# Performance work log

Hardware: AMD Instinct MI355X
Metric: run time of the kernel (lower is better)

Reference implementation:

```python
import jax, jax.numpy as jnp
import numpy as np

B, T, D, H = 512, 512, 128, 128


def setup_inputs() -> dict:
    key = jax.random.key(0)
    k1, k2, k3 = jax.random.split(key, 3)
    bound = 1.0 / np.sqrt(D)  # kaiming_uniform with a=sqrt(5) on [D,H]
    inp = {
        "input": jax.random.normal(k1, (B, T, D), dtype=jnp.float32),
        "mask": jnp.ones((B, T), dtype=jnp.int32),
        "Wt": jax.random.uniform(k2, (D, H), jnp.float32, -bound, bound),
        "Wx": jax.random.uniform(k3, (D, H), jnp.float32, -bound, bound),
        "rate": jnp.zeros((1,), jnp.float32) + 0.8,
    }
    return inp


def reference(input, mask, Wt, Wx, rate):
    b, t, d = input.shape
    # time decays: [t-1, t-2, ..., 0] + 1  -> shape [t]
    b_time_decays = jnp.arange(t - 1, -1, -1, dtype=input.dtype) + 1.0  # [T]

    # get_last_visit: pick features at last valid (mask==1) timestep per batch
    last_idx = jnp.sum(mask, axis=1).astype(jnp.int32) - 1            # [B]
    last_visit = jnp.take_along_axis(input, last_idx[:, None, None], axis=1)[:, 0]  # [B,D]

    q = last_visit @ Wt                                   # [B,H]
    k = jnp.einsum('btd,dh->bth', input, Wx)              # [B,T,H]
    dot_product = jnp.einsum('bh,bth->bt', q, k)          # [B,T]

    sig = jax.nn.sigmoid(dot_product)
    denominator = jax.nn.sigmoid(rate) * (
        jnp.log(2.72 + (1.0 - sig)) * b_time_decays[None, :]
    )
    e = jax.nn.relu(sig / denominator)

    e = jnp.where(mask == 0, -1e9, e)
    a = jax.nn.softmax(e, axis=1)                         # [B,T]
    v = jnp.einsum('bt,btd->bd', a, input)                # [B,D]
    return v, a
```

## Files before the change

kernel.cpp:

```cpp
#include <hip/hip_runtime.h>
#include <math.h>

constexpr int Bn = 512;
constexpr int Tn = 512;
constexpr int Dn = 128;
constexpr int Hn = 128;

__device__ __forceinline__ float rowsum16(float x) {
    int v;
    v = __float_as_int(x);
    x += __int_as_float(__builtin_amdgcn_update_dpp(0, v, 0x121, 0xF, 0xF, true));
    v = __float_as_int(x);
    x += __int_as_float(__builtin_amdgcn_update_dpp(0, v, 0x122, 0xF, 0xF, true));
    v = __float_as_int(x);
    x += __int_as_float(__builtin_amdgcn_update_dpp(0, v, 0x124, 0xF, 0xF, true));
    v = __float_as_int(x);
    x += __int_as_float(__builtin_amdgcn_update_dpp(0, v, 0x128, 0xF, 0xF, true));
    return x;
}

__global__ __launch_bounds__(128)
void compute_u_kernel(const float* __restrict__ input,
                      const int*   __restrict__ mask,
                      const float* __restrict__ Wt,
                      const float* __restrict__ Wx,
                      float* __restrict__ ws_u)
{
    const int b   = blockIdx.x;
    const int tid = threadIdx.x;
    const float* __restrict__ inb = input + (size_t)b * Tn * Dn;

    __shared__ float lvs[Dn];
    __shared__ float qs[Hn];
    __shared__ int   ired[2];

    const int4 m4 = ((const int4*)(mask + (size_t)b * Tn))[tid];
    int ms = m4.x + m4.y + m4.z + m4.w;
    #pragma unroll
    for (int off = 32; off > 0; off >>= 1) ms += __shfl_down(ms, off, 64);
    if ((tid & 63) == 0) ired[tid >> 6] = ms;
    __syncthreads();
    const int last_idx = ired[0] + ired[1] - 1;

    lvs[tid] = inb[(size_t)last_idx * Dn + tid];
    __syncthreads();

    float q = 0.f;
    #pragma unroll 16
    for (int d = 0; d < Dn; ++d) q = fmaf(lvs[d], Wt[d * Hn + tid], q);
    qs[tid] = q;
    __syncthreads();

    float u = 0.f;
    const float* wxr = Wx + tid * Hn;
    #pragma unroll 16
    for (int h = 0; h < Hn; ++h) u = fmaf(wxr[h], qs[h], u);
    ws_u[b * Dn + tid] = u;
}

constexpr int NT2 = 512;
constexpr int NW2 = NT2 / 64;
constexpr int HR  = Tn / 2;
constexpr int SW  = HR / 32;

__global__ __launch_bounds__(NT2, 4)
void attn_stream2(const float* __restrict__ input,
                  const int*   __restrict__ mask,
                  const float* __restrict__ ws_u,
                  const float* __restrict__ rate,
                  float* __restrict__ vpart,
                  float* __restrict__ lpart,
                  float* __restrict__ out_a)
{
    const int j    = blockIdx.x;
    const int b    = j >> 1;
    const int half = j & 1;
    const int tid  = threadIdx.x;
    const int lane = tid & 63;
    const int wid  = tid >> 6;
    const int seg  = tid & 15;
    const int rg   = tid >> 4;
    const int rbase = half * HR;
    const float4* __restrict__ in4 = (const float4*)(input + (size_t)b * Tn * Dn);

    __shared__ int   msk[HR];
    __shared__ float redl[NW2];
    __shared__ float vp[32 * 132];

    if (tid < HR) msk[tid] = mask[(size_t)b * Tn + rbase + tid];
    const float4 u4a = ((const float4*)(ws_u + b * Dn))[seg * 2];
    const float4 u4b = ((const float4*)(ws_u + b * Dn))[seg * 2 + 1];
    const float srate = 1.f / (1.f + __expf(-rate[0]));
    __syncthreads();

    float4 v0 = make_float4(0.f, 0.f, 0.f, 0.f);
    float4 v1 = make_float4(0.f, 0.f, 0.f, 0.f);
    float  lsum = 0.f;

    #pragma unroll
    for (int s = 0; s < SW; ++s) {
        const int rl  = s * 32 + rg;
        const int row = rbase + rl;
        const float4 x0 = in4[row * 32 + seg * 2];
        const float4 x1 = in4[row * 32 + seg * 2 + 1];
        float dot = x0.x * u4a.x + x0.y * u4a.y + x0.z * u4a.z + x0.w * u4a.w;
        dot = fmaf(x1.x, u4b.x, dot);
        dot = fmaf(x1.y, u4b.y, dot);
        dot = fmaf(x1.z, u4b.z, dot);
        dot = fmaf(x1.w, u4b.w, dot);
        dot = rowsum16(dot);
        const float sig = 1.f / (1.f + __expf(-dot));
        const float den = srate * (__logf(2.72f + (1.f - sig)) * (float)(Tn - row));
        const float e   = fmaxf(sig / den, 0.f);
        const float p   = msk[rl] ? __expf(e) : 0.f;
        v0.x = fmaf(p, x0.x, v0.x);
        v0.y = fmaf(p, x0.y, v0.y);
        v0.z = fmaf(p, x0.z, v0.z);
        v0.w = fmaf(p, x0.w, v0.w);
        v1.x = fmaf(p, x1.x, v1.x);
        v1.y = fmaf(p, x1.y, v1.y);
        v1.z = fmaf(p, x1.z, v1.z);
        v1.w = fmaf(p, x1.w, v1.w);
        if (seg == 0) { out_a[(size_t)b * Tn + row] = p; lsum += p; }
    }

    {
        float* vr = vp + rg * 132 + seg * 8;
        ((float4*)vr)[0] = v0;
        ((float4*)vr)[1] = v1;
    }
    float ls = lsum;
    #pragma unroll
    for (int off = 32; off > 0; off >>= 1) ls += __shfl_down(ls, off, 64);
    if (lane == 0) redl[wid] = ls;
    __syncthreads();

    if (tid < Dn) {
        float s = 0.f;
        #pragma unroll
        for (int r = 0; r < 32; ++r) s += vp[r * 132 + tid];
        vpart[(size_t)j * Dn + tid] = s;
    }
    if (tid == 0) {
        float l = 0.f;
        #pragma unroll
        for (int w = 0; w < NW2; ++w) l += redl[w];
        lpart[j] = l;
    }
}

__global__ __launch_bounds__(512)
void attn_finish(const float* __restrict__ vpart,
                 const float* __restrict__ lpart,
                 float* __restrict__ out_v,
                 float* __restrict__ out_a)
{
    const int b   = blockIdx.x;
    const int tid = threadIdx.x;
    const float invl = 1.f / (lpart[2 * b] + lpart[2 * b + 1]);
    out_a[(size_t)b * Tn + tid] *= invl;
    if (tid < Dn)
        out_v[(size_t)b * Dn + tid] =
            (vpart[(size_t)(2 * b) * Dn + tid] + vpart[(size_t)(2 * b + 1) * Dn + tid]) * invl;
}

extern "C" void kernel_launch(void* const* d_in, const int* in_sizes, int n_in,
                              void* d_out, int out_size, void* d_ws, size_t ws_size,
                              hipStream_t stream) {
    const float* input = (const float*)d_in[0];
    const int*   mask  = (const int*)d_in[1];
    const float* Wt    = (const float*)d_in[2];
    const float* Wx    = (const float*)d_in[3];
    const float* rate  = (const float*)d_in[4];

    float* out   = (float*)d_out;
    float* out_v = out;
    float* out_a = out + Bn * Dn;

    float* ws_u  = (float*)d_ws;
    float* vpart = ws_u + (size_t)Bn * Dn;
    float* lpart = vpart + (size_t)2 * Bn * Dn;

    compute_u_kernel<<<Bn, 128, 0, stream>>>(input, mask, Wt, Wx, ws_u);
    attn_stream2<<<2 * Bn, NT2, 0, stream>>>(input, mask, ws_u, rate, vpart, lpart, out_a);
    attn_finish<<<Bn, 512, 0, stream>>>(vpart, lpart, out_v, out_a);
}
```

Before: 37.60 us.

## Stream input rows into LDS via async global_load_lds with triple buffering

Replaces direct per-thread global float4 loads in the attention streaming kernel with asynchronous global-to-LDS loads. Each wave gets its own triple-buffered ring of 4-row chunks, managed with explicit vmcnt waits, so memory traffic overlaps with compute. Attention probabilities are staged in LDS and written to global in one coalesced pass at the end. The LDS footprint grows (about 48KB of staging per block), which may reduce occupancy at 4 blocks per CU, and the hand-written waitcnt sequencing is fragile.

```diff
diff --git a/kernel.cpp b/kernel.cpp
--- a/kernel.cpp
+++ b/kernel.cpp
@@ -58,34 +58,40 @@
     ws_u[b * Dn + tid] = u;
 }
 
-constexpr int NT2 = 512;
-constexpr int NW2 = NT2 / 64;
-constexpr int HR  = Tn / 2;
-constexpr int SW  = HR / 32;
+constexpr int NT2    = 512;
+constexpr int NW2    = NT2 / 64;
+constexpr int HR     = Tn / 2;
+constexpr int RPW    = HR / NW2;
+constexpr int CHROWS = 4;
+constexpr int NCH    = RPW / CHROWS;
+constexpr int CB     = 3;
+constexpr int CHB    = CHROWS * Dn * 4;
 
 __global__ __launch_bounds__(NT2, 4)
-void attn_stream2(const float* __restrict__ input,
-                  const int*   __restrict__ mask,
-                  const float* __restrict__ ws_u,
-                  const float* __restrict__ rate,
-                  float* __restrict__ vpart,
-                  float* __restrict__ lpart,
-                  float* __restrict__ out_a)
+void attn_stream_dma(const float* __restrict__ input,
+                     const int*   __restrict__ mask,
+                     const float* __restrict__ ws_u,
+                     const float* __restrict__ rate,
+                     float* __restrict__ vpart,
+                     float* __restrict__ lpart,
+                     float* __restrict__ out_a)
 {
-    const int j    = blockIdx.x;
-    const int b    = j >> 1;
-    const int half = j & 1;
-    const int tid  = threadIdx.x;
-    const int lane = tid & 63;
-    const int wid  = tid >> 6;
-    const int seg  = tid & 15;
-    const int rg   = tid >> 4;
+    const int j     = blockIdx.x;
+    const int b     = j >> 1;
+    const int half  = j & 1;
+    const int tid   = threadIdx.x;
+    const int lane  = tid & 63;
+    const int w     = tid >> 6;
+    const int seg   = lane & 15;
+    const int rslot = lane >> 4;
     const int rbase = half * HR;
-    const float4* __restrict__ in4 = (const float4*)(input + (size_t)b * Tn * Dn);
-
+    const float* __restrict__ inb = input + (size_t)b * Tn * Dn;
+
+    __shared__ float stream[NW2 * CB * CHROWS * Dn];
+    __shared__ float vp[32 * 132];
+    __shared__ float ps_l[HR];
     __shared__ int   msk[HR];
     __shared__ float redl[NW2];
-    __shared__ float vp[32 * 132];
 
     if (tid < HR) msk[tid] = mask[(size_t)b * Tn + rbase + tid];
     const float4 u4a = ((const float4*)(ws_u + b * Dn))[seg * 2];
@@ -93,16 +99,36 @@
     const float srate = 1.f / (1.f + __expf(-rate[0]));
     __syncthreads();
 
+    const char* gwave = (const char*)inb + (size_t)(rbase + w * RPW) * (Dn * 4) + lane * 16;
+    char*       lwave = (char*)stream + w * (CB * CHB);
+    auto issue = [&](int c) {
+        const char* g = gwave + c * CHB;
+        char*       l = lwave + (c % CB) * CHB;
+        __builtin_amdgcn_global_load_lds((const __attribute__((address_space(1))) void*)g,
+                                         (__attribute__((address_space(3))) void*)l, 16, 0, 0);
+        __builtin_amdgcn_global_load_lds((const __attribute__((address_space(1))) void*)(g + 1024),
+                                         (__attribute__((address_space(3))) void*)(l + 1024), 16, 0, 0);
+    };
+
+    issue(0); issue(1); issue(2);
+
     float4 v0 = make_float4(0.f, 0.f, 0.f, 0.f);
     float4 v1 = make_float4(0.f, 0.f, 0.f, 0.f);
     float  lsum = 0.f;
 
     #pragma unroll
-    for (int s = 0; s < SW; ++s) {
-        const int rl  = s * 32 + rg;
-        const int row = rbase + rl;
-        const float4 x0 = in4[row * 32 + seg * 2];
-        const float4 x1 = in4[row * 32 + seg * 2 + 1];
+    for (int c = 0; c < NCH; ++c) {
+        if (c < NCH - 2)      asm volatile("s_waitcnt vmcnt(4)" ::: "memory");
+        else if (c == NCH - 2) asm volatile("s_waitcnt vmcnt(2)" ::: "memory");
+        else                   asm volatile("s_waitcnt vmcnt(0)" ::: "memory");
+        __builtin_amdgcn_sched_barrier(0);
+
+        const float4* sf4 = (const float4*)(lwave + (c % CB) * CHB);
+        const float4 x0 = sf4[rslot * 32 + seg * 2];
+        const float4 x1 = sf4[rslot * 32 + seg * 2 + 1];
+
+        const int rloc = w * RPW + c * CHROWS + rslot;
+        const int row  = rbase + rloc;
         float dot = x0.x * u4a.x + x0.y * u4a.y + x0.z * u4a.z + x0.w * u4a.w;
         dot = fmaf(x1.x, u4b.x, dot);
         dot = fmaf(x1.y, u4b.y, dot);
@@ -112,7 +138,7 @@
         const float sig = 1.f / (1.f + __expf(-dot));
         const float den = srate * (__logf(2.72f + (1.f - sig)) * (float)(Tn - row));
         const float e   = fmaxf(sig / den, 0.f);
-        const float p   = msk[rl] ? __expf(e) : 0.f;
+        const float p   = msk[rloc] ? __expf(e) : 0.f;
         v0.x = fmaf(p, x0.x, v0.x);
         v0.y = fmaf(p, x0.y, v0.y);
         v0.z = fmaf(p, x0.z, v0.z);
@@ -121,18 +147,23 @@
         v1.y = fmaf(p, x1.y, v1.y);
         v1.z = fmaf(p, x1.z, v1.z);
         v1.w = fmaf(p, x1.w, v1.w);
-        if (seg == 0) { out_a[(size_t)b * Tn + row] = p; lsum += p; }
+        if (seg == 0) { ps_l[rloc] = p; lsum += p; }
+
+        if (c + CB < NCH) {
+            asm volatile("s_waitcnt lgkmcnt(0)" ::: "memory");
+            issue(c + CB);
+        }
     }
 
     {
-        float* vr = vp + rg * 132 + seg * 8;
+        float* vr = vp + (w * 4 + rslot) * 132 + seg * 8;
         ((float4*)vr)[0] = v0;
         ((float4*)vr)[1] = v1;
     }
     float ls = lsum;
     #pragma unroll
     for (int off = 32; off > 0; off >>= 1) ls += __shfl_down(ls, off, 64);
-    if (lane == 0) redl[wid] = ls;
+    if (lane == 0) redl[w] = ls;
     __syncthreads();
 
     if (tid < Dn) {
@@ -144,9 +175,10 @@
     if (tid == 0) {
         float l = 0.f;
         #pragma unroll
-        for (int w = 0; w < NW2; ++w) l += redl[w];
+        for (int wv = 0; wv < NW2; ++wv) l += redl[wv];
         lpart[j] = l;
     }
+    if (tid < HR) out_a[(size_t)b * Tn + rbase + tid] = ps_l[tid];
 }
 
 __global__ __launch_bounds__(512)
@@ -182,6 +214,6 @@
     float* lpart = vpart + (size_t)2 * Bn * Dn;
 
     compute_u_kernel<<<Bn, 128, 0, stream>>>(input, mask, Wt, Wx, ws_u);
-    attn_stream2<<<2 * Bn, NT2, 0, stream>>>(input, mask, ws_u, rate, vpart, lpart, out_a);
+    attn_stream_dma<<<2 * Bn, NT2, 0, stream>>>(input, mask, ws_u, rate, vpart, lpart, out_a);
     attn_finish<<<Bn, 512, 0, stream>>>(vpart, lpart, out_v, out_a);
 }
```

After: 39.69 us. 5.6% more time.
